# Kernel optimization log

Measured on AMD Instinct MI355X. Metric: run time of the kernel, lower is better.

Reference implementation:

```python
import jax, jax.numpy as jnp
import numpy as np

D_MODEL = 768
N_HEADS = 12
D_HEAD = 64
N_MEM = 3072
ALPHA = 0.1
EPS = 1e-5
W_SCALE = 0.02  # standard init scale so energies/grads stay well-conditioned


def setup_inputs() -> dict:
    key = jax.random.key(0)
    k0, k1, k2, k3 = jax.random.split(key, 4)
    B, S = 8, 1024
    x = jax.random.normal(k0, (B, S, D_MODEL), jnp.float32)
    gamma = jnp.ones((1,), jnp.float32)                      # scalar LN gamma (ET uses a single gamma)
    delta = jnp.zeros((D_MODEL,), jnp.float32)               # LN bias
    Wq = jax.random.normal(k1, (N_HEADS, D_HEAD, D_MODEL), jnp.float32) * W_SCALE
    Wk = jax.random.normal(k2, (N_HEADS, D_HEAD, D_MODEL), jnp.float32) * W_SCALE
    beta = jnp.ones((N_HEADS,), jnp.float32) / np.sqrt(D_HEAD)  # per-head beta init 1/sqrt(d_head)
    xi = jax.random.normal(k3, (N_MEM, D_MODEL), jnp.float32) * W_SCALE
    return {"x": x, "gamma": gamma, "delta": delta, "Wq": Wq, "Wk": Wk,
            "beta": beta, "xi": xi, "n_steps": 12}


def _total_energy(x, gamma, delta, Wq, Wk, beta, xi):
    # --- EnergyLayerNorm: g = dL/dx, E_ln = <x, g> - L ---
    mean = jnp.mean(x, axis=-1, keepdims=True)
    xm = x - mean
    var = jnp.mean(xm * xm, axis=-1, keepdims=True)
    std = jnp.sqrt(var + EPS)
    g = gamma * xm / std + delta                       # (B,S,D)
    L = jnp.sum(D_MODEL * gamma * std) + jnp.sum(delta * x)
    e_ln = jnp.sum(x * g) - L
    # --- EnergyAttention: E = -sum_{b,h,q} (1/beta_h) * logsumexp_k(beta_h * Q.K) ---
    q = jnp.einsum('bsd,hyd->bhsy', g, Wq)
    k = jnp.einsum('bsd,hyd->bhsy', g, Wk)
    A = jnp.einsum('bhqy,bhky->bhqk', q, k)            # (B,H,S,S)
    lse = jax.nn.logsumexp(beta[None, :, None, None] * A, axis=-1)  # (B,H,S)
    e_attn = -jnp.sum(lse / beta[None, :, None])
    # --- HopfieldNetwork: E = -1/2 sum relu(g @ xi^T)^2 ---
    h = jnp.einsum('bsd,md->bsm', g, xi)               # (B,S,M)
    e_hop = -0.5 * jnp.sum(jnp.square(jax.nn.relu(h)))
    return e_ln + e_attn + e_hop


def reference(x, gamma, delta, Wq, Wk, beta, xi, n_steps):
    grad_fn = jax.grad(_total_energy, argnums=0)

    def step(state, _):
        return state - ALPHA * grad_fn(state, gamma, delta, Wq, Wk, beta, xi), None

    final, _ = jax.lax.scan(step, x, None, length=n_steps)
    return final
```

## Files before the change

### kernel.cpp

```cpp
#include <hip/hip_runtime.h>
#include <hip/hip_bf16.h>
#include <stdint.h>

#define T_TOK 8192
#define DM    768
#define NH    12
#define DH    64
#define SEQ   1024
#define NBH   96
#define NMEM  3072
#define NUP   4608
#define ALPHA 0.1f
#define EPS   1e-5f
#define NSTEPS 12
#define PAD   72
#define SPLITK 3

typedef unsigned short us;
typedef __bf16 bf16x8 __attribute__((ext_vector_type(8)));
typedef float  f32x4  __attribute__((ext_vector_type(4)));

__device__ __forceinline__ us f2bf(float f) {
  uint32_t u = __builtin_bit_cast(uint32_t, f);
  u += 0x7fffu + ((u >> 16) & 1u);
  return (us)(u >> 16);
}

__device__ __forceinline__ f32x4 mfma16(bf16x8 a, bf16x8 b, f32x4 c) {
  return __builtin_amdgcn_mfma_f32_16x16x32_bf16(a, b, c, 0, 0, 0);
}

__device__ __forceinline__ void gld16(const void* g, void* l) {
  __builtin_amdgcn_global_load_lds(
      (const __attribute__((address_space(1))) void*)(uintptr_t)g,
      (__attribute__((address_space(3))) void*)(uint32_t)(uintptr_t)l,
      16, 0, 0);
}

__device__ __forceinline__ float block_sum(float v, float* sb, int tid) {
#pragma unroll
  for (int d = 32; d >= 1; d >>= 1) v += __shfl_xor(v, d);
  __syncthreads();
  if ((tid & 63) == 0) sb[tid >> 6] = v;
  __syncthreads();
  return sb[0] + sb[1] + sb[2] + sb[3];
}

__global__ __launch_bounds__(256) void pack_w(const float* __restrict__ Wq,
                                              const float* __restrict__ Wk,
                                              const float* __restrict__ xi,
                                              us* __restrict__ Wup, us* __restrict__ WdT) {
  int idx = blockIdx.x * 256 + threadIdx.x;
  if (idx >= NUP * DM) return;
  int r = idx / DM, d = idx - r * DM;
  float v = (r < 768) ? Wq[idx] : (r < 1536 ? Wk[idx - 768 * DM] : xi[idx - 1536 * DM]);
  us h = f2bf(v);
  Wup[idx] = h;
  WdT[(size_t)d * NUP + r] = h;
}

__global__ __launch_bounds__(256) void ln_fwd(const float* __restrict__ X,
                                              const float* __restrict__ gamma,
                                              const float* __restrict__ delta,
                                              us* __restrict__ g_bf,
                                              float* __restrict__ meanb, float* __restrict__ rstdb) {
  int t = blockIdx.x, tid = threadIdx.x;
  const float* x = X + (size_t)t * DM;
  __shared__ float sb[4];
  float v0 = x[tid], v1 = x[tid + 256], v2 = x[tid + 512];
  float mean = block_sum(v0 + v1 + v2, sb, tid) * (1.0f / DM);
  float d0 = v0 - mean, d1 = v1 - mean, d2 = v2 - mean;
  float var = block_sum(d0 * d0 + d1 * d1 + d2 * d2, sb, tid) * (1.0f / DM);
  float rstd = rsqrtf(var + EPS);
  float gm = gamma[0];
  us* go = g_bf + (size_t)t * DM;
  go[tid]       = f2bf(gm * d0 * rstd + delta[tid]);
  go[tid + 256] = f2bf(gm * d1 * rstd + delta[tid + 256]);
  go[tid + 512] = f2bf(gm * d2 * rstd + delta[tid + 512]);
  if (tid == 0) { meanb[t] = mean; rstdb[t] = rstd; }
}

template <int MODE>
__global__ __launch_bounds__(256) void gemm_bt(const us* __restrict__ A, const us* __restrict__ B,
                                               int Kstride, int kchunk, us* __restrict__ QKout,
                                               us* __restrict__ Dout, float* __restrict__ Gout) {
  __shared__ us As[128 * 32];
  __shared__ us Bs[128 * 32];
  int tid = threadIdx.x;
  int w = tid >> 6, lane = tid & 63, lm = lane & 15, lq = lane >> 4;
  int m0 = blockIdx.x * 128, n0 = blockIdx.y * 128;
  int wm = (w >> 1) * 64, wn = (w & 1) * 64;
  int kbeg = blockIdx.z * kchunk, kend = kbeg + kchunk;
  f32x4 zero = {0.f, 0.f, 0.f, 0.f};
  f32x4 acc[4][4];
#pragma unroll
  for (int i = 0; i < 4; i++)
#pragma unroll
    for (int j = 0; j < 4; j++) acc[i][j] = zero;

  const us* Ag = A + (size_t)(m0 + (tid >> 2)) * Kstride + (tid & 3) * 8;
  const us* Bg = B + (size_t)(n0 + (tid >> 2)) * Kstride + (tid & 3) * 8;
  us* lA = &As[tid * 8];
  us* lB = &Bs[tid * 8];
  const size_t half = (size_t)64 * Kstride;

  for (int k0 = kbeg; k0 < kend; k0 += 32) {
    __syncthreads();
    gld16(Ag + k0, lA);
    gld16(Ag + half + k0, lA + 2048);
    gld16(Bg + k0, lB);
    gld16(Bg + half + k0, lB + 2048);
    __syncthreads();
    bf16x8 af[4], bfr[4];
#pragma unroll
    for (int mt = 0; mt < 4; mt++) af[mt] = *(const bf16x8*)&As[(wm + mt * 16 + lm) * 32 + lq * 8];
#pragma unroll
    for (int nt = 0; nt < 4; nt++) bfr[nt] = *(const bf16x8*)&Bs[(wn + nt * 16 + lm) * 32 + lq * 8];
#pragma unroll
    for (int mt = 0; mt < 4; mt++)
#pragma unroll
      for (int nt = 0; nt < 4; nt++) acc[mt][nt] = mfma16(af[mt], bfr[nt], acc[mt][nt]);
  }
  float* Gz = (MODE == 1) ? Gout + (size_t)blockIdx.z * T_TOK * DM : nullptr;
#pragma unroll
  for (int mt = 0; mt < 4; mt++) {
    int row = m0 + wm + mt * 16 + lq * 4;
#pragma unroll
    for (int nt = 0; nt < 4; nt++) {
      int col = n0 + wn + nt * 16 + lm;
#pragma unroll
      for (int r = 0; r < 4; r++) {
        float v = acc[mt][nt][r];
        if (MODE == 0) {
          if (col < 1536) QKout[(size_t)(row + r) * 1536 + col] = f2bf(v);
          else            Dout[(size_t)(row + r) * NUP + col]   = f2bf(fmaxf(v, 0.f));
        } else {
          Gz[(size_t)(row + r) * DM + col] = v;
        }
      }
    }
  }
}

__global__ __launch_bounds__(256) void transpose_qk(const us* __restrict__ QK,
                                                    us* __restrict__ Qt, us* __restrict__ Kt) {
  int bh = blockIdx.x, kt = blockIdx.y, which = blockIdx.z;
  int b = bh / NH, h = bh - b * NH;
  int tid = threadIdx.x;
  __shared__ us tile[64][72];
  int c0 = h * 64 + (which ? 768 : 0);
  us* dst = (which ? Kt : Qt) + (size_t)bh * 64 * 1024;
#pragma unroll
  for (int r = 0; r < 2; r++) {
    int key = r * 32 + (tid >> 3); int yb = (tid & 7) * 8;
    *(bf16x8*)&tile[key][yb] =
        *(const bf16x8*)&QK[(size_t)(b * SEQ + kt * 64 + key) * 1536 + c0 + yb];
  }
  __syncthreads();
#pragma unroll
  for (int r = 0; r < 2; r++) {
    int lin = r * 256 + tid; int y = lin >> 3; int kb = (lin & 7) * 8;
    __align__(16) us tmp[8];
#pragma unroll
    for (int j = 0; j < 8; j++) tmp[j] = tile[kb + j][y];
    *(bf16x8*)&dst[(size_t)y * 1024 + kt * 64 + kb] = *(bf16x8*)tmp;
  }
}

__global__ __launch_bounds__(256) void attn_fwd(const us* __restrict__ QK, const us* __restrict__ Ktg,
                                                const float* __restrict__ beta,
                                                us* __restrict__ Dbuf, float* __restrict__ lse) {
  __shared__ us Qs[64 * PAD];
  __shared__ us Ks[64 * PAD];
  __shared__ us Kts[64 * PAD];
  __shared__ us Ps[4 * 16 * PAD];
  int bh = blockIdx.x, qt = blockIdx.y;
  int b = bh / NH, h = bh - b * NH;
  int tid = threadIdx.x, w = tid >> 6, lane = tid & 63, lm = lane & 15, lq = lane >> 4;
  float betah = beta[h];
#pragma unroll
  for (int r = 0; r < 2; r++) {
    int row = r * 32 + (tid >> 3); int yb = (tid & 7) * 8;
    *(bf16x8*)&Qs[row * PAD + yb] =
        *(const bf16x8*)&QK[(size_t)(b * SEQ + qt * 64 + row) * 1536 + h * 64 + yb];
  }
  __syncthreads();
  bf16x8 aq0 = *(const bf16x8*)&Qs[(w * 16 + lm) * PAD + lq * 8];
  bf16x8 aq1 = *(const bf16x8*)&Qs[(w * 16 + lm) * PAD + 32 + lq * 8];
  f32x4 zero = {0.f, 0.f, 0.f, 0.f};
  f32x4 O[4] = {zero, zero, zero, zero};
  float lacc[4] = {0.f, 0.f, 0.f, 0.f};
  us* pw = &Ps[w * 16 * PAD];

  for (int kc = 0; kc < SEQ; kc += 64) {
    __syncthreads();
#pragma unroll
    for (int r = 0; r < 2; r++) {
      int row = r * 32 + (tid >> 3); int yb = (tid & 7) * 8;
      *(bf16x8*)&Ks[row * PAD + yb] =
          *(const bf16x8*)&QK[(size_t)(b * SEQ + kc + row) * 1536 + 768 + h * 64 + yb];
      int lin = r * 256 + tid; int y = lin >> 3; int kb = (lin & 7) * 8;
      *(bf16x8*)&Kts[y * PAD + kb] =
          *(const bf16x8*)&Ktg[(size_t)(bh * 64 + y) * 1024 + kc + kb];
    }
    __syncthreads();
#pragma unroll
    for (int kk = 0; kk < 4; kk++) {
      f32x4 s = mfma16(aq0, *(const bf16x8*)&Ks[(kk * 16 + lm) * PAD + lq * 8], zero);
      s = mfma16(aq1, *(const bf16x8*)&Ks[(kk * 16 + lm) * PAD + 32 + lq * 8], s);
#pragma unroll
      for (int r = 0; r < 4; r++) {
        float p = __expf(betah * s[r]);
        lacc[r] += p;
        pw[(lq * 4 + r) * PAD + kk * 16 + lm] = f2bf(p);
      }
    }
    bf16x8 pa0 = *(const bf16x8*)&pw[lm * PAD + lq * 8];
    bf16x8 pa1 = *(const bf16x8*)&pw[lm * PAD + 32 + lq * 8];
#pragma unroll
    for (int nt = 0; nt < 4; nt++) {
      O[nt] = mfma16(pa0, *(const bf16x8*)&Kts[(nt * 16 + lm) * PAD + lq * 8], O[nt]);
      O[nt] = mfma16(pa1, *(const bf16x8*)&Kts[(nt * 16 + lm) * PAD + 32 + lq * 8], O[nt]);
    }
  }
  float l[4];
#pragma unroll
  for (int r = 0; r < 4; r++) {
    float v = lacc[r];
    v += __shfl_xor(v, 1); v += __shfl_xor(v, 2);
    v += __shfl_xor(v, 4); v += __shfl_xor(v, 8);
    l[r] = v;
  }
  float inv[4];
#pragma unroll
  for (int r = 0; r < 4; r++) inv[r] = 1.f / l[r];
#pragma unroll
  for (int nt = 0; nt < 4; nt++)
#pragma unroll
    for (int r = 0; r < 4; r++) {
      int q = qt * 64 + w * 16 + lq * 4 + r;
      Dbuf[(size_t)(b * SEQ + q) * NUP + h * 64 + nt * 16 + lm] = f2bf(O[nt][r] * inv[r]);
    }
  if (lm == 0) {
#pragma unroll
    for (int r = 0; r < 4; r++)
      lse[bh * SEQ + qt * 64 + w * 16 + lq * 4 + r] = __logf(l[r]);
  }
}

__global__ __launch_bounds__(256) void attn_bwd(const us* __restrict__ QK, const us* __restrict__ Qtg,
                                                const float* __restrict__ lse,
                                                const float* __restrict__ beta,
                                                us* __restrict__ Dbuf) {
  __shared__ us Ks2[64 * PAD];
  __shared__ us Qs2[64 * PAD];
  __shared__ us Qts[64 * PAD];
  __shared__ us Ps[4 * 16 * PAD];
  int bh = blockIdx.x, kt = blockIdx.y;
  int b = bh / NH, h = bh - b * NH;
  int tid = threadIdx.x, w = tid >> 6, lane = tid & 63, lm = lane & 15, lq = lane >> 4;
  float betah = beta[h];
#pragma unroll
  for (int r = 0; r < 2; r++) {
    int row = r * 32 + (tid >> 3); int yb = (tid & 7) * 8;
    *(bf16x8*)&Ks2[row * PAD + yb] =
        *(const bf16x8*)&QK[(size_t)(b * SEQ + kt * 64 + row) * 1536 + 768 + h * 64 + yb];
  }
  __syncthreads();
  bf16x8 ak0 = *(const bf16x8*)&Ks2[(w * 16 + lm) * PAD + lq * 8];
  bf16x8 ak1 = *(const bf16x8*)&Ks2[(w * 16 + lm) * PAD + 32 + lq * 8];
  f32x4 zero = {0.f, 0.f, 0.f, 0.f};
  f32x4 O[4] = {zero, zero, zero, zero};
  us* pw = &Ps[w * 16 * PAD];

  for (int qc = 0; qc < SEQ; qc += 64) {
    __syncthreads();
#pragma unroll
    for (int r = 0; r < 2; r++) {
      int row = r * 32 + (tid >> 3); int yb = (tid & 7) * 8;
      *(bf16x8*)&Qs2[row * PAD + yb] =
          *(const bf16x8*)&QK[(size_t)(b * SEQ + qc + row) * 1536 + h * 64 + yb];
      int lin = r * 256 + tid; int y = lin >> 3; int qb = (lin & 7) * 8;
      *(bf16x8*)&Qts[y * PAD + qb] =
          *(const bf16x8*)&Qtg[(size_t)(bh * 64 + y) * 1024 + qc + qb];
    }
    __syncthreads();
#pragma unroll
    for (int kk = 0; kk < 4; kk++) {
      f32x4 s = mfma16(ak0, *(const bf16x8*)&Qs2[(kk * 16 + lm) * PAD + lq * 8], zero);
      s = mfma16(ak1, *(const bf16x8*)&Qs2[(kk * 16 + lm) * PAD + 32 + lq * 8], s);
      float lv = lse[bh * SEQ + qc + kk * 16 + lm];
#pragma unroll
      for (int r = 0; r < 4; r++)
        pw[(lq * 4 + r) * PAD + kk * 16 + lm] = f2bf(__expf(betah * s[r] - lv));
    }
    bf16x8 pa0 = *(const bf16x8*)&pw[lm * PAD + lq * 8];
    bf16x8 pa1 = *(const bf16x8*)&pw[lm * PAD + 32 + lq * 8];
#pragma unroll
    for (int nt = 0; nt < 4; nt++) {
      O[nt] = mfma16(pa0, *(const bf16x8*)&Qts[(nt * 16 + lm) * PAD + lq * 8], O[nt]);
      O[nt] = mfma16(pa1, *(const bf16x8*)&Qts[(nt * 16 + lm) * PAD + 32 + lq * 8], O[nt]);
    }
  }
#pragma unroll
  for (int nt = 0; nt < 4; nt++)
#pragma unroll
    for (int r = 0; r < 4; r++) {
      int key = kt * 64 + w * 16 + lq * 4 + r;
      Dbuf[(size_t)(b * SEQ + key) * NUP + 768 + h * 64 + nt * 16 + lm] = f2bf(O[nt][r]);
    }
}

__global__ __launch_bounds__(256) void update_x(float* __restrict__ X, const float* __restrict__ G,
                                                float* __restrict__ meanb,
                                                float* __restrict__ rstdb,
                                                const float* __restrict__ gamma,
                                                const float* __restrict__ delta,
                                                us* __restrict__ g_bf) {
  int t = blockIdx.x, tid = threadIdx.x;
  __shared__ float sb[4];
  float mean = meanb[t], rstd = rstdb[t], gm = gamma[0];
  float* x = X + (size_t)t * DM;
  const float* g0 = G + (size_t)t * DM;
  const size_t GS = (size_t)T_TOK * DM;
  int i0 = tid, i1 = tid + 256, i2 = tid + 512;
  float x0 = x[i0], x1 = x[i1], x2 = x[i2];
  float gv0 = g0[i0] + g0[i0 + GS] + g0[i0 + 2 * GS];
  float gv1 = g0[i1] + g0[i1 + GS] + g0[i1 + 2 * GS];
  float gv2 = g0[i2] + g0[i2 + GS] + g0[i2 + 2 * GS];
  float v0 = x0 - gv0, v1 = x1 - gv1, v2 = x2 - gv2;
  float n0 = (x0 - mean) * rstd, n1 = (x1 - mean) * rstd, n2 = (x2 - mean) * rstd;
  float s1 = block_sum(v0 + v1 + v2, sb, tid) * (1.0f / DM);
  float s2 = block_sum(v0 * n0 + v1 * n1 + v2 * n2, sb, tid) * (1.0f / DM);
  float c = ALPHA * gm * rstd;
  float y0 = x0 - c * (v0 - s1 - n0 * s2);
  float y1 = x1 - c * (v1 - s1 - n1 * s2);
  float y2 = x2 - c * (v2 - s1 - n2 * s2);
  x[i0] = y0; x[i1] = y1; x[i2] = y2;
  float mean2 = block_sum(y0 + y1 + y2, sb, tid) * (1.0f / DM);
  float d0 = y0 - mean2, d1 = y1 - mean2, d2 = y2 - mean2;
  float var2 = block_sum(d0 * d0 + d1 * d1 + d2 * d2, sb, tid) * (1.0f / DM);
  float rstd2 = rsqrtf(var2 + EPS);
  us* go = g_bf + (size_t)t * DM;
  go[i0] = f2bf(gm * d0 * rstd2 + delta[i0]);
  go[i1] = f2bf(gm * d1 * rstd2 + delta[i1]);
  go[i2] = f2bf(gm * d2 * rstd2 + delta[i2]);
  if (tid == 0) { meanb[t] = mean2; rstdb[t] = rstd2; }
}

extern "C" void kernel_launch(void* const* d_in, const int* in_sizes, int n_in,
                              void* d_out, int out_size, void* d_ws, size_t ws_size,
                              hipStream_t stream) {
  const float* x_in  = (const float*)d_in[0];
  const float* gamma = (const float*)d_in[1];
  const float* delta = (const float*)d_in[2];
  const float* Wq    = (const float*)d_in[3];
  const float* Wk    = (const float*)d_in[4];
  const float* beta  = (const float*)d_in[5];
  const float* xi    = (const float*)d_in[6];
  float* X = (float*)d_out;

  char* p = (char*)d_ws;
  auto carve = [&](size_t bytes) -> char* {
    char* q = p; p += (bytes + 255) & ~(size_t)255; return q;
  };
  us*    g_bf  = (us*)carve((size_t)T_TOK * DM * 2);
  float* meanb = (float*)carve((size_t)T_TOK * 4);
  float* rstdb = (float*)carve((size_t)T_TOK * 4);
  us*    QK    = (us*)carve((size_t)T_TOK * 1536 * 2);
  us*    Qt    = (us*)carve((size_t)NBH * 64 * 1024 * 2);
  us*    Kt    = (us*)carve((size_t)NBH * 64 * 1024 * 2);
  float* lseb  = (float*)carve((size_t)NBH * SEQ * 4);
  us*    Dbuf  = (us*)carve((size_t)T_TOK * NUP * 2);
  float* G     = (float*)carve((size_t)SPLITK * T_TOK * DM * 4);
  us*    Wup   = (us*)carve((size_t)NUP * DM * 2);
  us*    WdT   = (us*)carve((size_t)DM * NUP * 2);

  hipMemcpyAsync(X, x_in, (size_t)T_TOK * DM * 4, hipMemcpyDeviceToDevice, stream);
  pack_w<<<(NUP * DM + 255) / 256, 256, 0, stream>>>(Wq, Wk, xi, Wup, WdT);
  ln_fwd<<<T_TOK, 256, 0, stream>>>(X, gamma, delta, g_bf, meanb, rstdb);

  for (int s = 0; s < NSTEPS; s++) {
    gemm_bt<0><<<dim3(64, 36, 1), 256, 0, stream>>>(g_bf, Wup, DM, DM, QK, Dbuf, nullptr);
    transpose_qk<<<dim3(NBH, 16, 2), 256, 0, stream>>>(QK, Qt, Kt);
    attn_fwd<<<dim3(NBH, 16), 256, 0, stream>>>(QK, Kt, beta, Dbuf, lseb);
    attn_bwd<<<dim3(NBH, 16), 256, 0, stream>>>(QK, Qt, lseb, beta, Dbuf);
    gemm_bt<1><<<dim3(64, 6, SPLITK), 256, 0, stream>>>(Dbuf, WdT, NUP, NUP / SPLITK,
                                                        nullptr, nullptr, G);
    update_x<<<T_TOK, 256, 0, stream>>>(X, G, meanb, rstdb, gamma, delta, g_bf);
  }
}
```

Baseline: 3.912 ms.

## Rewrite bf16 GEMM with 256x256 tiles, triple-buffered LDS pipeline and XCD remap

The GEMM kernel moves from 128x128 tiles with 4 waves and a single synchronous LDS buffer to 256x256 tiles with 8 waves. It adds a 3-stage async global-to-LDS prefetch using manual vmcnt waits, an XOR swizzle of the LDS layout to avoid bank conflicts, s_setprio around the MFMA blocks, and a block-id remap that spreads workgroups across XCDs. The aim is to hide memory latency and raise MFMA utilisation in the two projection GEMMs. In exchange, the larger tile gives far fewer workgroups (576 and 288) and higher register and LDS pressure, and the unrolled loop requires the K-tile count to be a multiple of 3.

```diff
diff --git a/kernel.cpp b/kernel.cpp
--- a/kernel.cpp
+++ b/kernel.cpp
@@ -81,53 +81,101 @@
 }
 
 template <int MODE>
-__global__ __launch_bounds__(256) void gemm_bt(const us* __restrict__ A, const us* __restrict__ B,
-                                               int Kstride, int kchunk, us* __restrict__ QKout,
-                                               us* __restrict__ Dout, float* __restrict__ Gout) {
-  __shared__ us As[128 * 32];
-  __shared__ us Bs[128 * 32];
+__global__ __launch_bounds__(512, 2) void gemm_bt(const us* __restrict__ A, const us* __restrict__ B,
+                                                  int Kstride, int kchunk, us* __restrict__ QKout,
+                                                  us* __restrict__ Dout, float* __restrict__ Gout) {
+  __shared__ us As[3 * 256 * 32];
+  __shared__ us Bs[3 * 256 * 32];
   int tid = threadIdx.x;
   int w = tid >> 6, lane = tid & 63, lm = lane & 15, lq = lane >> 4;
-  int m0 = blockIdx.x * 128, n0 = blockIdx.y * 128;
-  int wm = (w >> 1) * 64, wn = (w & 1) * 64;
-  int kbeg = blockIdx.z * kchunk, kend = kbeg + kchunk;
-  f32x4 zero = {0.f, 0.f, 0.f, 0.f};
-  f32x4 acc[4][4];
-#pragma unroll
-  for (int i = 0; i < 4; i++)
-#pragma unroll
-    for (int j = 0; j < 4; j++) acc[i][j] = zero;
-
-  const us* Ag = A + (size_t)(m0 + (tid >> 2)) * Kstride + (tid & 3) * 8;
-  const us* Bg = B + (size_t)(n0 + (tid >> 2)) * Kstride + (tid & 3) * 8;
-  us* lA = &As[tid * 8];
-  us* lB = &Bs[tid * 8];
-  const size_t half = (size_t)64 * Kstride;
-
-  for (int k0 = kbeg; k0 < kend; k0 += 32) {
-    __syncthreads();
-    gld16(Ag + k0, lA);
-    gld16(Ag + half + k0, lA + 2048);
-    gld16(Bg + k0, lB);
-    gld16(Bg + half + k0, lB + 2048);
-    __syncthreads();
-    bf16x8 af[4], bfr[4];
-#pragma unroll
-    for (int mt = 0; mt < 4; mt++) af[mt] = *(const bf16x8*)&As[(wm + mt * 16 + lm) * 32 + lq * 8];
-#pragma unroll
-    for (int nt = 0; nt < 4; nt++) bfr[nt] = *(const bf16x8*)&Bs[(wn + nt * 16 + lm) * 32 + lq * 8];
-#pragma unroll
-    for (int mt = 0; mt < 4; mt++)
-#pragma unroll
-      for (int nt = 0; nt < 4; nt++) acc[mt][nt] = mfma16(af[mt], bfr[nt], acc[mt][nt]);
-  }
+  int wm = w >> 2, wn = w & 3;
+
+  int nwg  = gridDim.x * gridDim.y;
+  int id   = blockIdx.y * gridDim.x + blockIdx.x;
+  int qq   = nwg >> 3, rr = nwg & 7;
+  int xcd  = id & 7, rank = id >> 3;
+  int nid  = (xcd < rr ? xcd * (qq + 1) : rr * (qq + 1) + (xcd - rr) * qq) + rank;
+  int bm   = nid % gridDim.x, bn = nid / gridDim.x;
+  int m0 = bm * 256, n0 = bn * 256;
+  int kbeg = blockIdx.z * kchunk;
+  int NT = kchunk >> 5;
+
+  int sr  = w * 16 + (lane >> 2);
+  int k8s = (lane & 3) ^ ((lane >> 3) & 3);
+  const us* pa = A + (size_t)(m0 + sr) * Kstride + kbeg + k8s * 8;
+  const us* pb = B + (size_t)(n0 + sr) * Kstride + kbeg + k8s * 8;
+  const size_t hstep = (size_t)128 * Kstride;
+  us* dA0 = &As[tid * 8];
+  us* dB0 = &Bs[tid * 8];
+
+  int kx   = (lq ^ ((lm >> 1) & 3)) * 8;
+  int aoff = (wm * 128 + lm) * 32 + kx;
+  int boff = (wn * 64  + lm) * 32 + kx;
+  const us* Ar = As + aoff;
+  const us* Br = Bs + boff;
+
+  f32x4 zero4 = {0.f, 0.f, 0.f, 0.f};
+  f32x4 acc[8][4];
+#pragma unroll
+  for (int i = 0; i < 8; i++)
+#pragma unroll
+    for (int j = 0; j < 4; j++) acc[i][j] = zero4;
+
+#define STAGE_A(S, T) { gld16(pa + (size_t)(T) * 32,         dA0 + (S) * 8192); \
+                        gld16(pa + (size_t)(T) * 32 + hstep, dA0 + (S) * 8192 + 4096); }
+#define STAGE_B(S, T) { gld16(pb + (size_t)(T) * 32,         dB0 + (S) * 8192); \
+                        gld16(pb + (size_t)(T) * 32 + hstep, dB0 + (S) * 8192 + 4096); }
+
+  STAGE_A(0, 0); STAGE_B(0, 0);
+  STAGE_A(1, 1); STAGE_B(1, 1);
+  asm volatile("s_waitcnt vmcnt(4)" ::: "memory");
+  __builtin_amdgcn_s_barrier();
+
+#define ITER(T, S) {                                                            \
+    bf16x8 af_[4], bf_[4];                                                      \
+    _Pragma("unroll") for (int x = 0; x < 4; x++)                               \
+      af_[x] = *(const bf16x8*)(Ar + (S) * 8192 + x * 512);                     \
+    _Pragma("unroll") for (int x = 0; x < 4; x++)                               \
+      bf_[x] = *(const bf16x8*)(Br + (S) * 8192 + x * 512);                     \
+    if ((T) + 2 < NT) STAGE_A(((S) + 2) % 3, (T) + 2);                          \
+    __builtin_amdgcn_s_barrier();                                               \
+    __builtin_amdgcn_s_setprio(1);                                              \
+    _Pragma("unroll") for (int mt = 0; mt < 4; mt++)                            \
+      _Pragma("unroll") for (int nt = 0; nt < 4; nt++)                          \
+        acc[mt][nt] = mfma16(af_[mt], bf_[nt], acc[mt][nt]);                    \
+    __builtin_amdgcn_s_setprio(0);                                              \
+    __builtin_amdgcn_s_barrier();                                               \
+    _Pragma("unroll") for (int x = 0; x < 4; x++)                               \
+      af_[x] = *(const bf16x8*)(Ar + (S) * 8192 + (x + 4) * 512);               \
+    if ((T) + 2 < NT) STAGE_B(((S) + 2) % 3, (T) + 2);                          \
+    __builtin_amdgcn_s_barrier();                                               \
+    __builtin_amdgcn_s_setprio(1);                                              \
+    _Pragma("unroll") for (int mt = 0; mt < 4; mt++)                            \
+      _Pragma("unroll") for (int nt = 0; nt < 4; nt++)                          \
+        acc[mt + 4][nt] = mfma16(af_[mt], bf_[nt], acc[mt + 4][nt]);            \
+    __builtin_amdgcn_s_setprio(0);                                              \
+    asm volatile("s_waitcnt lgkmcnt(0)" ::: "memory");                          \
+    if ((T) + 2 < NT)      { asm volatile("s_waitcnt vmcnt(4)" ::: "memory"); } \
+    else if ((T) + 1 < NT) { asm volatile("s_waitcnt vmcnt(0)" ::: "memory"); } \
+    __builtin_amdgcn_s_barrier();                                               \
+  }
+
+  for (int t = 0; t < NT; t += 3) {
+    ITER(t,     0);
+    ITER(t + 1, 1);
+    ITER(t + 2, 2);
+  }
+#undef ITER
+#undef STAGE_A
+#undef STAGE_B
+
   float* Gz = (MODE == 1) ? Gout + (size_t)blockIdx.z * T_TOK * DM : nullptr;
 #pragma unroll
-  for (int mt = 0; mt < 4; mt++) {
-    int row = m0 + wm + mt * 16 + lq * 4;
+  for (int mt = 0; mt < 8; mt++) {
+    int row = m0 + wm * 128 + mt * 16 + lq * 4;
 #pragma unroll
     for (int nt = 0; nt < 4; nt++) {
-      int col = n0 + wn + nt * 16 + lm;
+      int col = n0 + wn * 64 + nt * 16 + lm;
 #pragma unroll
       for (int r = 0; r < 4; r++) {
         float v = acc[mt][nt][r];
@@ -381,11 +429,11 @@
   ln_fwd<<<T_TOK, 256, 0, stream>>>(X, gamma, delta, g_bf, meanb, rstdb);
 
   for (int s = 0; s < NSTEPS; s++) {
-    gemm_bt<0><<<dim3(64, 36, 1), 256, 0, stream>>>(g_bf, Wup, DM, DM, QK, Dbuf, nullptr);
+    gemm_bt<0><<<dim3(32, 18, 1), 512, 0, stream>>>(g_bf, Wup, DM, DM, QK, Dbuf, nullptr);
     transpose_qk<<<dim3(NBH, 16, 2), 256, 0, stream>>>(QK, Qt, Kt);
     attn_fwd<<<dim3(NBH, 16), 256, 0, stream>>>(QK, Kt, beta, Dbuf, lseb);
     attn_bwd<<<dim3(NBH, 16), 256, 0, stream>>>(QK, Qt, lseb, beta, Dbuf);
-    gemm_bt<1><<<dim3(64, 6, SPLITK), 256, 0, stream>>>(Dbuf, WdT, NUP, NUP / SPLITK,
+    gemm_bt<1><<<dim3(32, 3, SPLITK), 512, 0, stream>>>(Dbuf, WdT, NUP, NUP / SPLITK,
                                                         nullptr, nullptr, G);
     update_x<<<T_TOK, 256, 0, stream>>>(X, G, meanb, rstdb, gamma, delta, g_bf);
   }
```

After: 3.890 ms. No clear change (-0.6%).
